# Optimization experiments

Measured on AMD Instinct MI355X. Metric: run time of the kernel, lower is better.

## Reference

```python
import jax, jax.numpy as jnp
import numpy as np

B, M, C = 32, 24564, 81
IGNORE = 0


def setup_inputs() -> dict:
    key = jax.random.key(0)
    k1, k2, k3, k4 = jax.random.split(key, 4)
    loc_preds = jax.random.normal(k1, (B, M, 4), dtype=jnp.float32)
    loc_targets = jax.random.normal(k2, (B, M, 4), dtype=jnp.float32)
    cls_preds = jax.random.normal(k3, (B, M, C), dtype=jnp.float32)
    cls_targets = jax.random.randint(k4, (B, M), 0, C, dtype=jnp.int64)
    return {"loc_preds": loc_preds, "loc_targets": loc_targets,
            "cls_preds": cls_preds, "cls_targets": cls_targets}


def _smooth_l1_sum(pred, target, mask):
    # F.smooth_l1_loss(beta=1, reduction='sum') over masked elements
    d = pred - target
    ad = jnp.abs(d)
    l = jnp.where(ad < 1.0, 0.5 * d * d, ad - 0.5)
    return jnp.sum(l * mask)


def reference(loc_preds, loc_targets, cls_preds, cls_targets):
    pos = cls_targets != IGNORE                      # [B, M] bool
    num_pos = jnp.sum(pos)                           # scalar int

    # localization loss over positive anchors only
    loc_loss = _smooth_l1_sum(loc_preds, loc_targets,
                              pos[..., None].astype(loc_preds.dtype))

    # per-anchor cross entropy
    logp = jax.nn.log_softmax(cls_preds, axis=-1)    # [B, M, C]
    ce = -jnp.take_along_axis(logp, cls_targets[..., None], axis=-1)[..., 0]
    # torch: cls_loss[cls_targets == ignore_class] = 0 (before mining)
    ce = jnp.where(pos, ce, jnp.zeros((), ce.dtype))  # [B, M]

    # hard negative mining (faithful double argsort, rank < 3*num_pos)
    masked = ce * (pos.astype(ce.dtype) - 1.0)        # [B, M]
    idx = jnp.argsort(masked, axis=1)
    rank = jnp.argsort(idx, axis=1)
    num_neg = 3 * jnp.sum(pos, axis=1)                # [B]
    neg = rank < num_neg[:, None]                     # [B, M] bool

    sel = (pos | neg).astype(ce.dtype)
    cls_loss = jnp.sum(ce * sel)

    denom = num_pos.astype(loc_loss.dtype)
    return loc_loss / denom, cls_loss / denom
```

## Files before the change

kernel.cpp:

```cpp
#include <hip/hip_runtime.h>
#include <math.h>

constexpr int kC     = 81;
constexpr int kCp    = 84;
constexpr int kN     = 32 * 24564;
constexpr int kTile  = 64;
constexpr int kTiles = kN / kTile;
constexpr int kLoads = 21;
constexpr int kGrid  = 768;

__device__ __forceinline__ void gload_lds16(const float* g, float* l) {
    __builtin_amdgcn_global_load_lds(
        (const __attribute__((address_space(1))) void*)g,
        (__attribute__((address_space(3))) void*)l,
        16, 0, 0);
}

__device__ __forceinline__ void stage(const float* __restrict__ cls_p,
                                      int tile, float* sb, int tid) {
    const float* gbase = cls_p + (size_t)tile * (kTile * kC);
    #pragma unroll
    for (int k = 0; k < kLoads; ++k) {
        const int id = k * 64 + tid;
        const int r  = id / 21;
        int c = (id - r * 21) * 4;
        if (c > 77) c = 77;
        gload_lds16(gbase + r * kC + c, sb + id * 4);
    }
}

__global__ __launch_bounds__(64) void ssd_kernel(
    const float* __restrict__ loc_p,
    const float* __restrict__ loc_t,
    const float* __restrict__ cls_p,
    const int*   __restrict__ tgt,
    float4* __restrict__ part)
{
    __shared__ float sbuf[2][kTile * kCp];

    const int tid = threadIdx.x;
    float lsum = 0.f, csum = 0.f, np = 0.f;

    int t  = blockIdx.x;
    int cb = 0;
    float4 p_cur = {0,0,0,0}, q_cur = {0,0,0,0};
    int    tg_cur = 0;

    {
        stage(cls_p, t, sbuf[0], tid);
        const int a = t * kTile + tid;
        p_cur  = reinterpret_cast<const float4*>(loc_p)[a];
        q_cur  = reinterpret_cast<const float4*>(loc_t)[a];
        tg_cur = tgt[a];
    }

    for (; t < kTiles; t += kGrid) {
        const int nt = t + kGrid;
        float4 p_nxt = {0,0,0,0}, q_nxt = {0,0,0,0};
        int    tg_nxt = 0;

        if (nt < kTiles) {
            stage(cls_p, nt, sbuf[cb ^ 1], tid);
            const int a = nt * kTile + tid;
            p_nxt  = reinterpret_cast<const float4*>(loc_p)[a];
            q_nxt  = reinterpret_cast<const float4*>(loc_t)[a];
            tg_nxt = tgt[a];
            asm volatile("s_waitcnt vmcnt(24)" ::: "memory");
        } else {
            asm volatile("s_waitcnt vmcnt(0)" ::: "memory");
        }

        {
            const float* row = &sbuf[cb][tid * kCp];
            const float4* __restrict__ r4 = reinterpret_cast<const float4*>(row);
            float s0 = 0.f, s1 = 0.f, s2 = 0.f, s3 = 0.f;
            #pragma unroll
            for (int c = 0; c < 20; ++c) {
                const float4 v = r4[c];
                s0 += __expf(v.x);
                s1 += __expf(v.y);
                s2 += __expf(v.z);
                s3 += __expf(v.w);
            }
            const float s = ((s0 + s1) + (s2 + s3)) + __expf(row[80]);
            const float mask = (tg_cur != 0) ? 1.f : 0.f;
            np   += mask;
            csum += mask * (__logf(s) - row[tg_cur]);

            float d, ad, l = 0.f;
            d = p_cur.x - q_cur.x; ad = fabsf(d); l += (ad < 1.f) ? 0.5f*d*d : ad - 0.5f;
            d = p_cur.y - q_cur.y; ad = fabsf(d); l += (ad < 1.f) ? 0.5f*d*d : ad - 0.5f;
            d = p_cur.z - q_cur.z; ad = fabsf(d); l += (ad < 1.f) ? 0.5f*d*d : ad - 0.5f;
            d = p_cur.w - q_cur.w; ad = fabsf(d); l += (ad < 1.f) ? 0.5f*d*d : ad - 0.5f;
            lsum += mask * l;
        }

        cb ^= 1;
        p_cur = p_nxt; q_cur = q_nxt; tg_cur = tg_nxt;
    }

    #pragma unroll
    for (int off = 32; off > 0; off >>= 1) {
        lsum += __shfl_down(lsum, off, 64);
        csum += __shfl_down(csum, off, 64);
        np   += __shfl_down(np,   off, 64);
    }
    if (tid == 0)
        part[blockIdx.x] = make_float4(lsum, csum, np, 0.f);
}

__global__ __launch_bounds__(256) void ssd_finalize(
    const float4* __restrict__ part, float* __restrict__ out)
{
    __shared__ float red[3][4];
    float l = 0.f, c = 0.f, n = 0.f;
    for (int i = threadIdx.x; i < kGrid; i += 256) {
        const float4 v = part[i];
        l += v.x; c += v.y; n += v.z;
    }
    #pragma unroll
    for (int off = 32; off > 0; off >>= 1) {
        l += __shfl_down(l, off, 64);
        c += __shfl_down(c, off, 64);
        n += __shfl_down(n, off, 64);
    }
    const int w = threadIdx.x >> 6;
    if ((threadIdx.x & 63) == 0) { red[0][w] = l; red[1][w] = c; red[2][w] = n; }
    __syncthreads();
    if (threadIdx.x == 0) {
        const float L = red[0][0] + red[0][1] + red[0][2] + red[0][3];
        const float C = red[1][0] + red[1][1] + red[1][2] + red[1][3];
        const float N = red[2][0] + red[2][1] + red[2][2] + red[2][3];
        out[0] = L / N;
        out[1] = C / N;
    }
}

extern "C" void kernel_launch(void* const* d_in, const int* in_sizes, int n_in,
                              void* d_out, int out_size, void* d_ws, size_t ws_size,
                              hipStream_t stream) {
    const float* loc_p = (const float*)d_in[0];
    const float* loc_t = (const float*)d_in[1];
    const float* cls_p = (const float*)d_in[2];
    const int*   tgt   = (const int*)d_in[3];
    float* out = (float*)d_out;

    float4* part = (float4*)d_ws;

    ssd_kernel<<<kGrid, 64, 0, stream>>>(loc_p, loc_t, cls_p, tgt, part);
    ssd_finalize<<<1, 256, 0, stream>>>(part, out);
}
```

Before: 52.29 us.

## Split each anchor's class row across two lanes with half-size tiles

Tiles shrink from 64 to 32 anchors, and each anchor's 81 logits are now summed by two lanes (low and high half of the wave), combined with a lane-xor shuffle. The grid grows to 1792 blocks, and the LDS row pitch is padded to 88 so the staging loads map cleanly, with the target index remapped for the last class. The aim is more blocks and shorter per-lane exp chains, to raise memory-level parallelism on a bandwidth-bound pass. The cost is half the lanes sitting idle during the loc-loss and CE epilogue, plus extra shuffle and staging overhead.

```diff
diff --git a/kernel.cpp b/kernel.cpp
--- a/kernel.cpp
+++ b/kernel.cpp
@@ -2,12 +2,12 @@
 #include <math.h>
 
 constexpr int kC     = 81;
-constexpr int kCp    = 84;
+constexpr int kCp    = 88;
+constexpr int kRows  = 32;
 constexpr int kN     = 32 * 24564;
-constexpr int kTile  = 64;
-constexpr int kTiles = kN / kTile;
-constexpr int kLoads = 21;
-constexpr int kGrid  = 768;
+constexpr int kTiles = kN / kRows;
+constexpr int kLoads = 11;
+constexpr int kGrid  = 1792;
 
 __device__ __forceinline__ void gload_lds16(const float* g, float* l) {
     __builtin_amdgcn_global_load_lds(
@@ -18,12 +18,12 @@
 
 __device__ __forceinline__ void stage(const float* __restrict__ cls_p,
                                       int tile, float* sb, int tid) {
-    const float* gbase = cls_p + (size_t)tile * (kTile * kC);
+    const float* gbase = cls_p + (size_t)tile * (kRows * kC);
     #pragma unroll
     for (int k = 0; k < kLoads; ++k) {
         const int id = k * 64 + tid;
-        const int r  = id / 21;
-        int c = (id - r * 21) * 4;
+        const int r  = id / 22;
+        int c = (id - r * 22) * 4;
         if (c > 77) c = 77;
         gload_lds16(gbase + r * kC + c, sb + id * 4);
     }
@@ -36,9 +36,11 @@
     const int*   __restrict__ tgt,
     float4* __restrict__ part)
 {
-    __shared__ float sbuf[2][kTile * kCp];
+    __shared__ float sbuf[2][kRows * kCp];
 
     const int tid = threadIdx.x;
+    const int l   = tid & 31;
+    const bool lo = tid < 32;
     float lsum = 0.f, csum = 0.f, np = 0.f;
 
     int t  = blockIdx.x;
@@ -46,9 +48,9 @@
     float4 p_cur = {0,0,0,0}, q_cur = {0,0,0,0};
     int    tg_cur = 0;
 
-    {
-        stage(cls_p, t, sbuf[0], tid);
-        const int a = t * kTile + tid;
+    stage(cls_p, t, sbuf[0], tid);
+    if (lo) {
+        const int a = t * kRows + l;
         p_cur  = reinterpret_cast<const float4*>(loc_p)[a];
         q_cur  = reinterpret_cast<const float4*>(loc_t)[a];
         tg_cur = tgt[a];
@@ -61,38 +63,52 @@
 
         if (nt < kTiles) {
             stage(cls_p, nt, sbuf[cb ^ 1], tid);
-            const int a = nt * kTile + tid;
-            p_nxt  = reinterpret_cast<const float4*>(loc_p)[a];
-            q_nxt  = reinterpret_cast<const float4*>(loc_t)[a];
-            tg_nxt = tgt[a];
-            asm volatile("s_waitcnt vmcnt(24)" ::: "memory");
+            if (lo) {
+                const int a = nt * kRows + l;
+                p_nxt  = reinterpret_cast<const float4*>(loc_p)[a];
+                q_nxt  = reinterpret_cast<const float4*>(loc_t)[a];
+                tg_nxt = tgt[a];
+            }
+            asm volatile("s_waitcnt vmcnt(14)" ::: "memory");
         } else {
             asm volatile("s_waitcnt vmcnt(0)" ::: "memory");
         }
 
         {
-            const float* row = &sbuf[cb][tid * kCp];
+            const float* row = &sbuf[cb][l * kCp];
             const float4* __restrict__ r4 = reinterpret_cast<const float4*>(row);
+            const int base = lo ? 0 : 9;
             float s0 = 0.f, s1 = 0.f, s2 = 0.f, s3 = 0.f;
             #pragma unroll
-            for (int c = 0; c < 20; ++c) {
-                const float4 v = r4[c];
-                s0 += __expf(v.x);
-                s1 += __expf(v.y);
-                s2 += __expf(v.z);
-                s3 += __expf(v.w);
+            for (int c = 0; c < 9; ++c) {
+                const float4 v = r4[base + c];
+                s0 += __expf(v.x); s1 += __expf(v.y);
+                s2 += __expf(v.z); s3 += __expf(v.w);
             }
-            const float s = ((s0 + s1) + (s2 + s3)) + __expf(row[80]);
-            const float mask = (tg_cur != 0) ? 1.f : 0.f;
-            np   += mask;
-            csum += mask * (__logf(s) - row[tg_cur]);
+            float s = (s0 + s1) + (s2 + s3);
+            if (!lo) {
+                const float4 v = r4[18];
+                const float4 w = r4[19];
+                const float  z = r4[20].w;
+                s += __expf(v.x) + __expf(v.y) + __expf(v.z) + __expf(v.w)
+                   + __expf(w.x) + __expf(w.y) + __expf(w.z) + __expf(w.w)
+                   + __expf(z);
+            }
+            s += __shfl_xor(s, 32, 64);
 
-            float d, ad, l = 0.f;
-            d = p_cur.x - q_cur.x; ad = fabsf(d); l += (ad < 1.f) ? 0.5f*d*d : ad - 0.5f;
-            d = p_cur.y - q_cur.y; ad = fabsf(d); l += (ad < 1.f) ? 0.5f*d*d : ad - 0.5f;
-            d = p_cur.z - q_cur.z; ad = fabsf(d); l += (ad < 1.f) ? 0.5f*d*d : ad - 0.5f;
-            d = p_cur.w - q_cur.w; ad = fabsf(d); l += (ad < 1.f) ? 0.5f*d*d : ad - 0.5f;
-            lsum += mask * l;
+            if (lo) {
+                const float mask = (tg_cur != 0) ? 1.f : 0.f;
+                const int   ti   = (tg_cur == 80) ? 83 : tg_cur;
+                np   += mask;
+                csum += mask * (__logf(s) - row[ti]);
+
+                float d, ad, ll = 0.f;
+                d = p_cur.x - q_cur.x; ad = fabsf(d); ll += (ad < 1.f) ? 0.5f*d*d : ad - 0.5f;
+                d = p_cur.y - q_cur.y; ad = fabsf(d); ll += (ad < 1.f) ? 0.5f*d*d : ad - 0.5f;
+                d = p_cur.z - q_cur.z; ad = fabsf(d); ll += (ad < 1.f) ? 0.5f*d*d : ad - 0.5f;
+                d = p_cur.w - q_cur.w; ad = fabsf(d); ll += (ad < 1.f) ? 0.5f*d*d : ad - 0.5f;
+                lsum += mask * ll;
+            }
         }
 
         cb ^= 1;
```

Measured after the change: 51.35 us. About the same (-1.8%).
